# Optimization experiments

Hardware: AMD Instinct MI355X
Metric: run time of the kernel (lower is better)

## Reference

```python
import jax, jax.numpy as jnp
import numpy as np

DIM = 768
NUM_HEADS = 12
HEAD_DIM = DIM // NUM_HEADS
MAX_H = 32
MAX_W = 32


def setup_inputs() -> dict:
    key = jax.random.key(0)
    ks = jax.random.split(key, 7)
    B, H, W = 2, MAX_H, MAX_W
    N = H * W
    x = jax.random.normal(ks[0], (B, N, DIM), dtype=jnp.float32)
    qkv_w = jax.random.normal(ks[1], (3 * DIM, DIM), dtype=jnp.float32) * 0.02
    qkv_b = jax.random.normal(ks[2], (3 * DIM,), dtype=jnp.float32) * 0.02
    proj_w = jax.random.normal(ks[3], (DIM, DIM), dtype=jnp.float32) * 0.02
    proj_b = jax.random.normal(ks[4], (DIM,), dtype=jnp.float32) * 0.02
    rel_pos_h = jax.random.normal(ks[5], (2 * MAX_H - 1, HEAD_DIM), dtype=jnp.float32) * 0.02
    rel_pos_w = jax.random.normal(ks[6], (2 * MAX_W - 1, HEAD_DIM), dtype=jnp.float32) * 0.02
    return {"x": x, "qkv_w": qkv_w, "qkv_b": qkv_b, "proj_w": proj_w,
            "proj_b": proj_b, "rel_pos_h": rel_pos_h, "rel_pos_w": rel_pos_w,
            "x_h": H, "x_w": W}


def _rel_index(q_size, k_size):
    # q_size == k_size here (x_hw == max_hw), ratios are 1 and _interpolate is identity
    dist = jnp.arange(q_size)[:, None] - jnp.arange(k_size)[None, :] + (k_size - 1)
    return dist  # values in [0, 2*k_size-2]


def reference(x, qkv_w, qkv_b, proj_w, proj_b, rel_pos_h, rel_pos_w, x_h, x_w):
    B, N, dim = x.shape
    nh, hd = NUM_HEADS, HEAD_DIM
    qkv = (x @ qkv_w.T + qkv_b).reshape(B, N, 3, nh, hd)
    q, k, v = qkv[:, :, 0], qkv[:, :, 1], qkv[:, :, 2]  # [B, N, nh, hd]

    Rh = rel_pos_h[_rel_index(x_h, x_h)]  # [qh, kh, hd]
    Rw = rel_pos_w[_rel_index(x_w, x_w)]  # [qw, kw, hd]
    q2d = q.reshape(B, x_h, x_w, nh, hd)
    rel_h = jnp.einsum('bhwnc,hkc->bnhwk', q2d, Rh)  # [B, nh, qh, qw, kh]
    rel_w = jnp.einsum('bhwnc,wkc->bnhwk', q2d, Rw)  # [B, nh, qh, qw, kw]
    bias = (rel_h[..., :, None] + rel_w[..., None, :]).reshape(B, nh, N, N)

    scale = 1.0 / np.sqrt(hd).astype(np.float32)
    scores = jnp.einsum('bqhd,bkhd->bhqk', q, k) * scale + bias
    attn = jax.nn.softmax(scores, axis=-1)
    out = jnp.einsum('bhqk,bkhd->bqhd', attn, v).reshape(B, N, dim)
    return out @ proj_w.T + proj_b
```

## Files before the change

### kernel.cpp

```cpp
#include <hip/hip_runtime.h>

typedef float fx4 __attribute__((ext_vector_type(4)));
typedef float fx2 __attribute__((ext_vector_type(2)));
typedef short bfrag __attribute__((ext_vector_type(8)));
typedef float ffrag __attribute__((ext_vector_type(4)));
typedef unsigned short ush;

#define NTOK  1024
#define NHEADS 12
#define HD    64
#define DIMM  768

__device__ __forceinline__ float b2f(ush u) {
  union { unsigned i; float f; } x; x.i = ((unsigned)u) << 16; return x.f;
}
__device__ __forceinline__ ush f2b(float f) {
  union { float f; unsigned i; } x; x.f = f;
  unsigned r = x.i + 0x7fff + ((x.i >> 16) & 1);
  return (ush)(r >> 16);
}

__device__ __forceinline__ void gload16(const void* g, void* l) {
  __builtin_amdgcn_global_load_lds(
      (const __attribute__((address_space(1))) unsigned*)g,
      (__attribute__((address_space(3))) unsigned*)l, 16, 0, 0);
}

__device__ __forceinline__ ffrag mfma16(bfrag a, bfrag b, ffrag c) {
  return __builtin_amdgcn_mfma_f32_16x16x32_bf16(a, b, c, 0, 0, 0);
}

template<int N> __device__ __forceinline__ void vwait() {
  if constexpr (N == 0)      asm volatile("s_waitcnt vmcnt(0)" ::: "memory");
  else if constexpr (N == 1) asm volatile("s_waitcnt vmcnt(1)" ::: "memory");
  else if constexpr (N == 2) asm volatile("s_waitcnt vmcnt(2)" ::: "memory");
  else if constexpr (N == 3) asm volatile("s_waitcnt vmcnt(3)" ::: "memory");
  else if constexpr (N == 4) asm volatile("s_waitcnt vmcnt(4)" ::: "memory");
  else if constexpr (N == 6) asm volatile("s_waitcnt vmcnt(6)" ::: "memory");
  else if constexpr (N == 8) asm volatile("s_waitcnt vmcnt(8)" ::: "memory");
  else                       asm volatile("s_waitcnt vmcnt(12)" ::: "memory");
}
__device__ __forceinline__ void bar() {
  asm volatile("" ::: "memory");
  __builtin_amdgcn_s_barrier();
  asm volatile("" ::: "memory");
}
__device__ __forceinline__ void barL() {
  asm volatile("s_waitcnt lgkmcnt(0)" ::: "memory");
  __builtin_amdgcn_s_barrier();
  asm volatile("" ::: "memory");
}

__device__ __forceinline__ int swz(int row, int b) {
  return row * 128 + (b ^ ((row & 7) << 4));
}

__global__ __launch_bounds__(256) void k_cvt3(
    const float* __restrict__ x, const float* __restrict__ w,
    const float* __restrict__ pw,
    ush* __restrict__ xh, ush* __restrict__ xl,
    ush* __restrict__ wh,
    ush* __restrict__ pwh, ush* __restrict__ pwl)
{
  int i = blockIdx.x * 256 + threadIdx.x;
  const float* src; ush *h, *l; int off;
  bool wlo = true;
  if (i < 393216)      { src = x;  h = xh;  l = xl;  off = i; }
  else if (i < 835584) { src = w;  h = wh;  l = nullptr; wlo = false; off = i - 393216; }
  else                 { src = pw; h = pwh; l = pwl; off = i - 835584; }
  fx4 v = *(const fx4*)(src + (size_t)off * 4);
  ushort4 hh, ll;
  float t;
  hh.x = f2b(v[0]); t = v[0] - b2f(hh.x); ll.x = f2b(t);
  hh.y = f2b(v[1]); t = v[1] - b2f(hh.y); ll.y = f2b(t);
  hh.z = f2b(v[2]); t = v[2] - b2f(hh.z); ll.z = f2b(t);
  hh.w = f2b(v[3]); t = v[3] - b2f(hh.w); ll.w = f2b(t);
  *(ushort4*)(h + (size_t)off * 4) = hh;
  if (wlo) *(ushort4*)(l + (size_t)off * 4) = ll;
}

template<int MR, int NR, int NTERM>
__device__ __forceinline__ void gemm_pipe(
    const ush* __restrict__ Ah, const ush* __restrict__ Al,
    const ush* __restrict__ Bh, const ush* __restrict__ Bl,
    int row0, int col0, int K, short* lds, ffrag (&acc)[MR][NR])
{
  constexpr int F = (NTERM == 3) ? 4 * (MR + NR) : (4 * MR + 2 * NR);
  constexpr int LPS = F / 4;
  static_assert(F % 4 == 0, "frag count must be divisible by wave count");
  const int tid = threadIdx.x;
  const int lane = tid & 63, w = tid >> 6;
  const int wr = w >> 1, wc = w & 1;
  const int l15 = lane & 15, l8 = (lane >> 4) * 8;

  auto stage = [&](short* buf, int k0) {
    #pragma unroll
    for (int i = 0; i < LPS; i++) {
      int f = i * 4 + w;
      const ush* src;
      if (f < 2 * MR)
        src = Ah + (size_t)(row0 + f * 16 + l15) * K + k0 + l8;
      else if (f < 4 * MR)
        src = Al + (size_t)(row0 + (f - 2 * MR) * 16 + l15) * K + k0 + l8;
      else if (f < 4 * MR + 2 * NR)
        src = Bh + (size_t)(col0 + (f - 4 * MR) * 16 + l15) * K + k0 + l8;
      else
        src = Bl + (size_t)(col0 + (f - 4 * MR - 2 * NR) * 16 + l15) * K + k0 + l8;
      gload16(src, buf + f * 512);
    }
  };

  auto step = [&](const short* buf) {
    bfrag ah[MR], al[MR], bh[NR];
    #pragma unroll
    for (int i = 0; i < MR; i++) {
      ah[i] = *(const bfrag*)(buf + (wr * MR + i) * 512 + lane * 8);
      al[i] = *(const bfrag*)(buf + (2 * MR + wr * MR + i) * 512 + lane * 8);
    }
    #pragma unroll
    for (int j = 0; j < NR; j++)
      bh[j] = *(const bfrag*)(buf + (4 * MR + wc * NR + j) * 512 + lane * 8);
    if constexpr (NTERM == 3) {
      bfrag bl[NR];
      #pragma unroll
      for (int j = 0; j < NR; j++)
        bl[j] = *(const bfrag*)(buf + (4 * MR + 2 * NR + wc * NR + j) * 512 + lane * 8);
      #pragma unroll
      for (int i = 0; i < MR; i++)
        #pragma unroll
        for (int j = 0; j < NR; j++) {
          acc[i][j] = mfma16(ah[i], bh[j], acc[i][j]);
          acc[i][j] = mfma16(ah[i], bl[j], acc[i][j]);
          acc[i][j] = mfma16(al[i], bh[j], acc[i][j]);
        }
    } else {
      #pragma unroll
      for (int i = 0; i < MR; i++)
        #pragma unroll
        for (int j = 0; j < NR; j++) {
          acc[i][j] = mfma16(ah[i], bh[j], acc[i][j]);
          acc[i][j] = mfma16(al[i], bh[j], acc[i][j]);
        }
    }
  };

  const int nt = K / 32;
  stage(lds, 0);
  for (int t = 0; t < nt; t++) {
    bar();
    if (t + 1 < nt) {
      stage(lds + ((t + 1) & 1) * F * 512, (t + 1) * 32);
      vwait<LPS>();
    } else {
      vwait<0>();
    }
    bar();
    step(lds + (t & 1) * F * 512);
  }
}

__global__ __launch_bounds__(256) void k_qkv_mfma(
    const ush* __restrict__ xh, const ush* __restrict__ xl,
    const ush* __restrict__ wh,
    const float* __restrict__ bias,
    ush* __restrict__ qo, ush* __restrict__ ko, ush* __restrict__ vo)
{
  __shared__ short lds[2 * 24 * 512];
  const int orig = blockIdx.x;
  const int xcd = orig & 7, local = orig >> 3;
  const int lm = local & 3, ln = local >> 2;
  const int bm = (xcd & 3) * 4 + lm;
  const int bn = (xcd >> 2) * 9 + ln;
  const int row0 = bm * 128, col0 = bn * 128;
  ffrag acc[4][4] = {};
  gemm_pipe<4, 4, 2>(xh, xl, wh, wh, row0, col0, 768, lds, acc);

  const int tid = threadIdx.x, lane = tid & 63, w = tid >> 6;
  const int wr = w >> 1, wc = w & 1;
  const int l15 = lane & 15, l4 = lane >> 4;
  const int which = col0 / 768;
  const int base_head = (col0 - which * 768) >> 6;
  const int head = base_head + wc;
  ush* base = which == 0 ? qo : (which == 1 ? ko : vo);
  #pragma unroll
  for (int mi = 0; mi < 4; mi++)
    #pragma unroll
    for (int ni = 0; ni < 4; ni++) {
      int d = ni * 16 + l15;
      float bv = bias[col0 + wc * 64 + d];
      #pragma unroll
      for (int r = 0; r < 4; r++) {
        int row = row0 + wr * 64 + mi * 16 + l4 * 4 + r;
        int bb = row >> 10, n = row & 1023;
        base[((size_t)(bb * NHEADS + head) * NTOK + n) * HD + d] =
            f2b(acc[mi][ni][r] + bv);
      }
    }
}

__global__ __launch_bounds__(256) void k_proj_mfma(
    const ush* __restrict__ ah, const ush* __restrict__ al,
    const ush* __restrict__ bh, const ush* __restrict__ bl,
    const float* __restrict__ bias, float* __restrict__ out)
{
  __shared__ short lds[2 * 16 * 512];
  const int orig = blockIdx.x;
  const int xcd = orig & 7, local = orig >> 3;
  const int lm = local & 7, ln = local >> 3;
  const int bm = (xcd & 3) * 8 + lm;
  const int bn = (xcd >> 2) * 6 + ln;
  const int row0 = bm * 64, col0 = bn * 64;
  ffrag acc[2][2] = {};
  gemm_pipe<2, 2, 3>(ah, al, bh, bl, row0, col0, 768, lds, acc);

  const int tid = threadIdx.x, lane = tid & 63, w = tid >> 6;
  const int wr = w >> 1, wc = w & 1;
  const int l15 = lane & 15, l4 = lane >> 4;
  #pragma unroll
  for (int mi = 0; mi < 2; mi++)
    #pragma unroll
    for (int ni = 0; ni < 2; ni++) {
      int col = col0 + wc * 32 + ni * 16 + l15;
      float bv = bias[col];
      #pragma unroll
      for (int r = 0; r < 4; r++) {
        int row = row0 + wr * 32 + mi * 16 + l4 * 4 + r;
        out[(size_t)row * 768 + col] = acc[mi][ni][r] + bv;
      }
    }
}

__global__ __launch_bounds__(256) void k_rel(
    const ush* __restrict__ qT, const float* __restrict__ rph,
    const float* __restrict__ rpw,
    float* __restrict__ relh, float* __restrict__ relw)
{
  __shared__ float Qs[32][68];
  __shared__ float RhS[32][68];
  __shared__ float RwS[63][68];
  const int bid = blockIdx.x;
  const int pair = bid >> 5;
  const int nt = bid & 31;
  const int nbase = nt * 32;
  const ush* qp = qT + (size_t)pair * NTOK * HD + (size_t)nbase * HD;
  const int tid = threadIdx.x;
  #pragma unroll
  for (int ii = 0; ii < 2; ii++) {
    int f = ii * 256 + tid;
    int r = f >> 4, k4 = f & 15;
    ushort4 t = *(const ushort4*)(qp + (size_t)r * HD + k4 * 4);
    Qs[r][k4*4+0] = b2f(t.x); Qs[r][k4*4+1] = b2f(t.y);
    Qs[r][k4*4+2] = b2f(t.z); Qs[r][k4*4+3] = b2f(t.w);
    *(fx4*)&RhS[r][k4*4] = *(const fx4*)(rph + (size_t)(nt + r) * 64 + k4 * 4);
  }
  #pragma unroll
  for (int ii = 0; ii < 4; ii++) {
    int f = ii * 256 + tid;
    if (f < 1008) {
      int r = f >> 4, k4 = f & 15;
      *(fx4*)&RwS[r][k4*4] = *(const fx4*)(rpw + (size_t)r * 64 + k4 * 4);
    }
  }
  __syncthreads();
  const int nl = tid >> 3, rem = tid & 7;
  #pragma unroll
  for (int rep = 0; rep < 8; rep++) {
    int kidx = rep * 8 + rem;
    int hw = kidx >> 5;
    int k = kidx & 31;
    const float* rrow = hw ? &RwS[nl + 31 - k][0] : &RhS[31 - k][0];
    float sum = 0.f;
    #pragma unroll
    for (int c4 = 0; c4 < 16; c4++) {
      fx4 q = *(const fx4*)&Qs[nl][c4*4];
      fx4 rv = *(const fx4*)&rrow[c4*4];
      sum = fmaf(q[0], rv[0], sum);
      sum = fmaf(q[1], rv[1], sum);
      sum = fmaf(q[2], rv[2], sum);
      sum = fmaf(q[3], rv[3], sum);
    }
    float* dst = (hw ? relw : relh) + (size_t)pair * NTOK * 32 + (size_t)(nbase + nl) * 32 + k;
    *dst = sum;
  }
}

__global__ __launch_bounds__(256, 3) void k_attn_mfma(
    const ush* __restrict__ qT, const ush* __restrict__ kT,
    const ush* __restrict__ vT,
    const float* __restrict__ relh, const float* __restrict__ relw,
    ush* __restrict__ oph, ush* __restrict__ opl, float* __restrict__ ml)
{
  __shared__ short Kf[2 * 8 * 512];
  __shared__ char VTb[8192];
  __shared__ char Phb[8192];
  __shared__ char Plb[8192];
  __shared__ float RhS[64][36];

  const int orig = blockIdx.x;
  const int bid = (orig & 7) * 96 + (orig >> 3);
  const int ks   = bid & 1;
  const int qt   = (bid >> 1) & 15;
  const int pair = bid >> 5;
  const int q0 = qt * 64;
  const ush* qp = qT + (size_t)pair * NTOK * HD;
  const ush* kp = kT + (size_t)pair * NTOK * HD;
  const ush* vp = vT + (size_t)pair * NTOK * HD;
  const float* rhp = relh + (size_t)pair * NTOK * 32;
  const float* rwp = relw + (size_t)pair * NTOK * 32;

  const int tid = threadIdx.x;
  const int lane = tid & 63, w = tid >> 6;
  const int l15 = lane & 15, l4 = lane >> 4;
  const int wq = w * 16;
  const int kv = tid & 63, db = tid >> 6;

  auto issueK = [&](int tt) {
    const int gt = ks * 8 + tt;
    const ush* s0 = kp + (size_t)(gt * 64 + wq + l15) * HD + l4 * 8;
    short* dst = Kf + (tt & 1) * 4096 + (w * 2) * 512;
    gload16(s0, dst);
    gload16(s0 + 32, dst + 512);
  };
  auto issueV = [&](int tt, ushort4 (&vr)[4]) {
    const int gt = ks * 8 + tt;
    #pragma unroll
    for (int j = 0; j < 4; j++)
      vr[j] = *(const ushort4*)(vp + (size_t)(gt * 64 + kv) * HD + db * 16 + j * 4);
  };
  auto writeVT = [&](ushort4 (&vr)[4]) {
    #pragma unroll
    for (int j = 0; j < 4; j++) {
      int d0 = db * 16 + j * 4;
      *(ush*)(VTb + swz(d0 + 0, 2 * kv)) = vr[j].x;
      *(ush*)(VTb + swz(d0 + 1, 2 * kv)) = vr[j].y;
      *(ush*)(VTb + swz(d0 + 2, 2 * kv)) = vr[j].z;
      *(ush*)(VTb + swz(d0 + 3, 2 * kv)) = vr[j].w;
    }
  };

  {
    int row = tid >> 2, seg = tid & 3;
    const float* src = rhp + (size_t)(q0 + row) * 32 + seg * 8;
    *(fx4*)&RhS[row][seg * 8]     = *(const fx4*)src;
    *(fx4*)&RhS[row][seg * 8 + 4] = *(const fx4*)(src + 4);
  }
  bfrag qf[2];
  qf[0] = *(const bfrag*)(qp + (size_t)(q0 + wq + l15) * HD + l4 * 8);
  qf[1] = *(const bfrag*)(qp + (size_t)(q0 + wq + l15) * HD + 32 + l4 * 8);
  float rw[4][2];
  #pragma unroll
  for (int r = 0; r < 4; r++)
    #pragma unroll
    for (int h = 0; h < 2; h++)
      rw[r][h] = rwp[(size_t)(q0 + wq + l4 * 4 + r) * 32 + h * 16 + l15];

  asm volatile("" ::: "memory");
  ushort4 vrA[4], vrB[4];
  issueK(0); issueV(0, vrA); issueV(1, vrB);

  ffrag o[4] = {};
  float mrow[4] = {-3e38f, -3e38f, -3e38f, -3e38f};
  float lrow[4] = {};

  for (int tt = 0; tt < 8; tt++) {
    const int t = ks * 8 + tt;
    if (tt < 7) vwait<4>(); else vwait<0>();
    barL();

    if ((tt & 1) == 0) {
      writeVT(vrA);
      if (tt < 7) issueK(tt + 1);
      if (tt < 6) issueV(tt + 2, vrA);
    } else {
      writeVT(vrB);
      if (tt < 7) issueK(tt + 1);
      if (tt < 6) issueV(tt + 2, vrB);
    }

    const short* kbuf = Kf + (tt & 1) * 4096;
    ffrag s[4] = {};
    #pragma unroll
    for (int kf = 0; kf < 4; kf++) {
      bfrag kf0 = *(const bfrag*)(kbuf + (kf * 2 + 0) * 512 + lane * 8);
      bfrag kf1 = *(const bfrag*)(kbuf + (kf * 2 + 1) * 512 + lane * 8);
      s[kf] = mfma16(qf[0], kf0, s[kf]);
      s[kf] = mfma16(qf[1], kf1, s[kf]);
    }

    fx2 rh2[4];
    #pragma unroll
    for (int r = 0; r < 4; r++)
      rh2[r] = *(const fx2*)&RhS[wq + l4 * 4 + r][2 * t];
    float pm[4] = {-3e38f, -3e38f, -3e38f, -3e38f};
    #pragma unroll
    for (int kf = 0; kf < 4; kf++)
      #pragma unroll
      for (int r = 0; r < 4; r++) {
        float sc = fmaf(s[kf][r], 0.125f, rh2[r][kf >> 1] + rw[r][kf & 1]);
        s[kf][r] = sc;
        pm[r] = fmaxf(pm[r], sc);
      }
    #pragma unroll
    for (int off = 1; off < 16; off <<= 1)
      #pragma unroll
      for (int r = 0; r < 4; r++)
        pm[r] = fmaxf(pm[r], __shfl_xor(pm[r], off));
    float al[4], ps[4] = {0.f, 0.f, 0.f, 0.f};
    #pragma unroll
    for (int r = 0; r < 4; r++) {
      float mnew = fmaxf(mrow[r], pm[r]);
      al[r] = __expf(mrow[r] - mnew);
      mrow[r] = mnew;
    }
    #pragma unroll
    for (int kf = 0; kf < 4; kf++)
      #pragma unroll
      for (int r = 0; r < 4; r++) {
        float p = __expf(s[kf][r] - mrow[r]);
        s[kf][r] = p;
        ps[r] += p;
      }
    #pragma unroll
    for (int off = 1; off < 16; off <<= 1)
      #pragma unroll
      for (int r = 0; r < 4; r++)
        ps[r] += __shfl_xor(ps[r], off);
    #pragma unroll
    for (int r = 0; r < 4; r++)
      lrow[r] = fmaf(lrow[r], al[r], ps[r]);

    #pragma unroll
    for (int kf = 0; kf < 4; kf++)
      #pragma unroll
      for (int r = 0; r < 4; r++) {
        ush hi = f2b(s[kf][r]);
        float lo = s[kf][r] - b2f(hi);
        int a = swz(wq + l4 * 4 + r, kf * 32 + 2 * l15);
        *(ush*)(Phb + a) = hi;
        *(ush*)(Plb + a) = f2b(lo);
      }
    #pragma unroll
    for (int df = 0; df < 4; df++)
      #pragma unroll
      for (int r = 0; r < 4; r++)
        o[df][r] *= al[r];

    barL();

    bfrag ph[2], pl[2];
    #pragma unroll
    for (int kc = 0; kc < 2; kc++) {
      int a = swz(wq + l15, kc * 64 + l4 * 16);
      ph[kc] = *(const bfrag*)(Phb + a);
      pl[kc] = *(const bfrag*)(Plb + a);
    }
    #pragma unroll
    for (int df = 0; df < 4; df++)
      #pragma unroll
      for (int kc = 0; kc < 2; kc++) {
        bfrag vf = *(const bfrag*)(VTb + swz(df * 16 + l15, kc * 64 + l4 * 16));
        o[df] = mfma16(ph[kc], vf, o[df]);
        o[df] = mfma16(pl[kc], vf, o[df]);
      }
  }

  const int part = ((pair << 4) | qt) * 2 + ks;
  if (l15 == 0) {
    float* mlp = ml + (size_t)part * 128;
    #pragma unroll
    for (int r = 0; r < 4; r++) {
      int row = wq + l4 * 4 + r;
      mlp[row] = mrow[r];
      mlp[64 + row] = lrow[r];
    }
  }
  const size_t pbase = (size_t)part * 4096;
  #pragma unroll
  for (int df = 0; df < 4; df++)
    #pragma unroll
    for (int r = 0; r < 4; r++) {
      float val = o[df][r];
      int row = wq + l4 * 4 + r;
      size_t idx = pbase + (size_t)row * 64 + df * 16 + l15;
      ush hi = f2b(val);
      oph[idx] = hi;
      opl[idx] = f2b(val - b2f(hi));
    }
}

__global__ __launch_bounds__(256) void k_attn_merge(
    const ush* __restrict__ oph, const ush* __restrict__ opl,
    const float* __restrict__ ml,
    ush* __restrict__ o1h, ush* __restrict__ o1l)
{
  const int pq = blockIdx.x;
  const int pair = pq >> 4, qt = pq & 15;
  const int bb = pair / NHEADS, head = pair % NHEADS;
  __shared__ float M0[64], L0[64], M1[64], L1[64];
  const int tid = threadIdx.x;
  const float* mlp = ml + (size_t)pq * 256;
  if (tid < 64) {
    M0[tid] = mlp[tid];        L0[tid] = mlp[64 + tid];
    M1[tid] = mlp[128 + tid];  L1[tid] = mlp[192 + tid];
  }
  __syncthreads();
  const size_t b0 = (size_t)(pq * 2) * 4096;
  const size_t b1 = b0 + 4096;
  #pragma unroll
  for (int e = 0; e < 4; e++) {
    int q4 = e * 256 + tid;
    int row = q4 >> 4;
    int d4 = (q4 & 15) * 4;
    float m0 = M0[row], l0v = L0[row], m1 = M1[row], l1v = L1[row];
    float m = fmaxf(m0, m1);
    float a0 = __expf(m0 - m), a1 = __expf(m1 - m);
    float inv = 1.0f / (l0v * a0 + l1v * a1);
    ushort4 h0 = *(const ushort4*)(oph + b0 + (size_t)q4 * 4);
    ushort4 g0 = *(const ushort4*)(opl + b0 + (size_t)q4 * 4);
    ushort4 h1 = *(const ushort4*)(oph + b1 + (size_t)q4 * 4);
    ushort4 g1 = *(const ushort4*)(opl + b1 + (size_t)q4 * 4);
    float v0 = ((b2f(h0.x)+b2f(g0.x))*a0 + (b2f(h1.x)+b2f(g1.x))*a1) * inv;
    float v1 = ((b2f(h0.y)+b2f(g0.y))*a0 + (b2f(h1.y)+b2f(g1.y))*a1) * inv;
    float v2 = ((b2f(h0.z)+b2f(g0.z))*a0 + (b2f(h1.z)+b2f(g1.z))*a1) * inv;
    float v3 = ((b2f(h0.w)+b2f(g0.w))*a0 + (b2f(h1.w)+b2f(g1.w))*a1) * inv;
    size_t gidx = ((size_t)(bb * NTOK + qt * 64 + row)) * DIMM + head * HD + d4;
    ushort4 oh, ol;
    oh.x = f2b(v0); ol.x = f2b(v0 - b2f(oh.x));
    oh.y = f2b(v1); ol.y = f2b(v1 - b2f(oh.y));
    oh.z = f2b(v2); ol.z = f2b(v2 - b2f(oh.z));
    oh.w = f2b(v3); ol.w = f2b(v3 - b2f(oh.w));
    *(ushort4*)(o1h + gidx) = oh;
    *(ushort4*)(o1l + gidx) = ol;
  }
}

extern "C" void kernel_launch(void* const* d_in, const int* in_sizes, int n_in,
                              void* d_out, int out_size, void* d_ws, size_t ws_size,
                              hipStream_t stream)
{
  const float* x      = (const float*)d_in[0];
  const float* qkv_w  = (const float*)d_in[1];
  const float* qkv_b  = (const float*)d_in[2];
  const float* proj_w = (const float*)d_in[3];
  const float* proj_b = (const float*)d_in[4];
  const float* rph    = (const float*)d_in[5];
  const float* rpw    = (const float*)d_in[6];

  char* p = (char*)d_ws;
  ush* xh  = (ush*)p; p += 3145728;
  ush* xl  = (ush*)p; p += 3145728;
  ush* wh  = (ush*)p; p += 3538944;
  ush* wl  = (ush*)p; p += 3538944;
  ush* pwh = (ush*)p; p += 1179648;
  ush* pwl = (ush*)p; p += 1179648;
  ush* qb  = (ush*)p; p += 3145728;
  ush* kb  = (ush*)p; p += 3145728;
  ush* vb  = (ush*)p; p += 3145728;
  float* relh = (float*)p; p += 3145728;
  float* relw = (float*)p; p += 3145728;
  float* ml   = (float*)p; p += 393216;
  (void)wl;
  ush* oph = xh;
  ush* opl = wh;
  ush* o1h = qb;
  ush* o1l = kb;
  float* out = (float*)d_out;

  k_cvt3<<<dim3(3840), dim3(256), 0, stream>>>(x, qkv_w, proj_w,
                                               xh, xl, wh, pwh, pwl);
  k_qkv_mfma<<<dim3(288), dim3(256), 0, stream>>>(xh, xl, wh, qkv_b, qb, kb, vb);
  k_rel<<<dim3(768), dim3(256), 0, stream>>>(qb, rph, rpw, relh, relw);
  k_attn_mfma<<<dim3(768), dim3(256), 0, stream>>>(qb, kb, vb, relh, relw, oph, opl, ml);
  k_attn_merge<<<dim3(384), dim3(256), 0, stream>>>(oph, opl, ml, o1h, o1l);
  k_proj_mfma<<<dim3(384), dim3(256), 0, stream>>>(o1h, o1l, pwh, pwl, proj_b, out);
}
```

Before: 120.9 us.

## Replace LDS-staged GEMM pipeline with direct global-to-register double buffering

Removes the shared-memory staging and barriers from the QKV and projection GEMMs. Each wave now loads its own MFMA fragments straight from global memory into registers, double-buffered across K steps. This drops LDS traffic and the two barriers per step. In exchange, operand data that waves previously shared through LDS is now fetched redundantly from global memory or L2, and register pressure rises.

```diff
diff --git a/kernel.cpp b/kernel.cpp
--- a/kernel.cpp
+++ b/kernel.cpp
@@ -31,14 +31,10 @@
 }
 
 template<int N> __device__ __forceinline__ void vwait() {
-  if constexpr (N == 0)      asm volatile("s_waitcnt vmcnt(0)" ::: "memory");
-  else if constexpr (N == 1) asm volatile("s_waitcnt vmcnt(1)" ::: "memory");
-  else if constexpr (N == 2) asm volatile("s_waitcnt vmcnt(2)" ::: "memory");
-  else if constexpr (N == 3) asm volatile("s_waitcnt vmcnt(3)" ::: "memory");
-  else if constexpr (N == 4) asm volatile("s_waitcnt vmcnt(4)" ::: "memory");
-  else if constexpr (N == 6) asm volatile("s_waitcnt vmcnt(6)" ::: "memory");
-  else if constexpr (N == 8) asm volatile("s_waitcnt vmcnt(8)" ::: "memory");
-  else                       asm volatile("s_waitcnt vmcnt(12)" ::: "memory");
+  if constexpr (N == 0)       asm volatile("s_waitcnt vmcnt(0)" ::: "memory");
+  else if constexpr (N == 4)  asm volatile("s_waitcnt vmcnt(4)" ::: "memory");
+  else if constexpr (N == 6)  asm volatile("s_waitcnt vmcnt(6)" ::: "memory");
+  else                        asm volatile("s_waitcnt vmcnt(8)" ::: "memory");
 }
 __device__ __forceinline__ void bar() {
   asm volatile("" ::: "memory");
@@ -79,152 +75,136 @@
   if (wlo) *(ushort4*)(l + (size_t)off * 4) = ll;
 }
 
-template<int MR, int NR, int NTERM>
-__device__ __forceinline__ void gemm_pipe(
-    const ush* __restrict__ Ah, const ush* __restrict__ Al,
-    const ush* __restrict__ Bh, const ush* __restrict__ Bl,
-    int row0, int col0, int K, short* lds, ffrag (&acc)[MR][NR])
-{
-  constexpr int F = (NTERM == 3) ? 4 * (MR + NR) : (4 * MR + 2 * NR);
-  constexpr int LPS = F / 4;
-  static_assert(F % 4 == 0, "frag count must be divisible by wave count");
-  const int tid = threadIdx.x;
-  const int lane = tid & 63, w = tid >> 6;
-  const int wr = w >> 1, wc = w & 1;
-  const int l15 = lane & 15, l8 = (lane >> 4) * 8;
-
-  auto stage = [&](short* buf, int k0) {
-    #pragma unroll
-    for (int i = 0; i < LPS; i++) {
-      int f = i * 4 + w;
-      const ush* src;
-      if (f < 2 * MR)
-        src = Ah + (size_t)(row0 + f * 16 + l15) * K + k0 + l8;
-      else if (f < 4 * MR)
-        src = Al + (size_t)(row0 + (f - 2 * MR) * 16 + l15) * K + k0 + l8;
-      else if (f < 4 * MR + 2 * NR)
-        src = Bh + (size_t)(col0 + (f - 4 * MR) * 16 + l15) * K + k0 + l8;
-      else
-        src = Bl + (size_t)(col0 + (f - 4 * MR - 2 * NR) * 16 + l15) * K + k0 + l8;
-      gload16(src, buf + f * 512);
-    }
-  };
-
-  auto step = [&](const short* buf) {
-    bfrag ah[MR], al[MR], bh[NR];
-    #pragma unroll
-    for (int i = 0; i < MR; i++) {
-      ah[i] = *(const bfrag*)(buf + (wr * MR + i) * 512 + lane * 8);
-      al[i] = *(const bfrag*)(buf + (2 * MR + wr * MR + i) * 512 + lane * 8);
-    }
-    #pragma unroll
-    for (int j = 0; j < NR; j++)
-      bh[j] = *(const bfrag*)(buf + (4 * MR + wc * NR + j) * 512 + lane * 8);
-    if constexpr (NTERM == 3) {
-      bfrag bl[NR];
-      #pragma unroll
-      for (int j = 0; j < NR; j++)
-        bl[j] = *(const bfrag*)(buf + (4 * MR + 2 * NR + wc * NR + j) * 512 + lane * 8);
-      #pragma unroll
-      for (int i = 0; i < MR; i++)
-        #pragma unroll
-        for (int j = 0; j < NR; j++) {
-          acc[i][j] = mfma16(ah[i], bh[j], acc[i][j]);
-          acc[i][j] = mfma16(ah[i], bl[j], acc[i][j]);
-          acc[i][j] = mfma16(al[i], bh[j], acc[i][j]);
-        }
-    } else {
-      #pragma unroll
-      for (int i = 0; i < MR; i++)
-        #pragma unroll
-        for (int j = 0; j < NR; j++) {
-          acc[i][j] = mfma16(ah[i], bh[j], acc[i][j]);
-          acc[i][j] = mfma16(al[i], bh[j], acc[i][j]);
-        }
-    }
-  };
-
-  const int nt = K / 32;
-  stage(lds, 0);
-  for (int t = 0; t < nt; t++) {
-    bar();
-    if (t + 1 < nt) {
-      stage(lds + ((t + 1) & 1) * F * 512, (t + 1) * 32);
-      vwait<LPS>();
-    } else {
-      vwait<0>();
-    }
-    bar();
-    step(lds + (t & 1) * F * 512);
-  }
-}
-
 __global__ __launch_bounds__(256) void k_qkv_mfma(
     const ush* __restrict__ xh, const ush* __restrict__ xl,
     const ush* __restrict__ wh,
     const float* __restrict__ bias,
     ush* __restrict__ qo, ush* __restrict__ ko, ush* __restrict__ vo)
 {
-  __shared__ short lds[2 * 24 * 512];
   const int orig = blockIdx.x;
   const int xcd = orig & 7, local = orig >> 3;
   const int lm = local & 3, ln = local >> 2;
   const int bm = (xcd & 3) * 4 + lm;
   const int bn = (xcd >> 2) * 9 + ln;
-  const int row0 = bm * 128, col0 = bn * 128;
-  ffrag acc[4][4] = {};
-  gemm_pipe<4, 4, 2>(xh, xl, wh, wh, row0, col0, 768, lds, acc);
-
   const int tid = threadIdx.x, lane = tid & 63, w = tid >> 6;
   const int wr = w >> 1, wc = w & 1;
+  const int row0 = bm * 128 + wr * 64;
+  const int col0 = bn * 128 + wc * 64;
   const int l15 = lane & 15, l4 = lane >> 4;
+  const int K = 768;
+
+  const ush* pa[4]; const ush* pl[4]; const ush* pb[4];
+  #pragma unroll
+  for (int i = 0; i < 4; i++) {
+    size_t ro = (size_t)(row0 + i * 16 + l15) * K + l4 * 8;
+    size_t co = (size_t)(col0 + i * 16 + l15) * K + l4 * 8;
+    pa[i] = xh + ro; pl[i] = xl + ro; pb[i] = wh + co;
+  }
+
+  bfrag A0[4], L0[4], B0[4], A1[4], L1[4], B1[4];
+  ffrag acc[4][4] = {};
+
+#define LOADQ(A, L, B)                                          \
+  { _Pragma("unroll") for (int i = 0; i < 4; i++) {             \
+      A[i] = *(const bfrag*)pa[i]; pa[i] += 32;                 \
+      L[i] = *(const bfrag*)pl[i]; pl[i] += 32;                 \
+      B[i] = *(const bfrag*)pb[i]; pb[i] += 32; } }
+#define STEPQ(A, L, B)                                          \
+  { _Pragma("unroll") for (int i = 0; i < 4; i++)               \
+      _Pragma("unroll") for (int j = 0; j < 4; j++) {           \
+        acc[i][j] = mfma16(A[i], B[j], acc[i][j]);              \
+        acc[i][j] = mfma16(L[i], B[j], acc[i][j]); } }
+
+  LOADQ(A0, L0, B0);
+  for (int t = 0; t < 24; t += 2) {
+    LOADQ(A1, L1, B1);
+    STEPQ(A0, L0, B0);
+    if (t + 2 < 24) LOADQ(A0, L0, B0);
+    STEPQ(A1, L1, B1);
+  }
+#undef LOADQ
+#undef STEPQ
+
   const int which = col0 / 768;
-  const int base_head = (col0 - which * 768) >> 6;
-  const int head = base_head + wc;
-  ush* base = which == 0 ? qo : (which == 1 ? ko : vo);
+  const int head  = (col0 - which * 768) >> 6;
+  ush* basep = which == 0 ? qo : (which == 1 ? ko : vo);
   #pragma unroll
   for (int mi = 0; mi < 4; mi++)
     #pragma unroll
     for (int ni = 0; ni < 4; ni++) {
       int d = ni * 16 + l15;
-      float bv = bias[col0 + wc * 64 + d];
+      float bv = bias[col0 + d];
       #pragma unroll
       for (int r = 0; r < 4; r++) {
-        int row = row0 + wr * 64 + mi * 16 + l4 * 4 + r;
+        int row = row0 + mi * 16 + l4 * 4 + r;
         int bb = row >> 10, n = row & 1023;
-        base[((size_t)(bb * NHEADS + head) * NTOK + n) * HD + d] =
+        basep[((size_t)(bb * NHEADS + head) * NTOK + n) * HD + d] =
             f2b(acc[mi][ni][r] + bv);
       }
     }
 }
 
 __global__ __launch_bounds__(256) void k_proj_mfma(
-    const ush* __restrict__ ah, const ush* __restrict__ al,
-    const ush* __restrict__ bh, const ush* __restrict__ bl,
+    const ush* __restrict__ ah_, const ush* __restrict__ al_,
+    const ush* __restrict__ bh_, const ush* __restrict__ bl_,
     const float* __restrict__ bias, float* __restrict__ out)
 {
-  __shared__ short lds[2 * 16 * 512];
   const int orig = blockIdx.x;
   const int xcd = orig & 7, local = orig >> 3;
   const int lm = local & 7, ln = local >> 3;
   const int bm = (xcd & 3) * 8 + lm;
   const int bn = (xcd >> 2) * 6 + ln;
-  const int row0 = bm * 64, col0 = bn * 64;
-  ffrag acc[2][2] = {};
-  gemm_pipe<2, 2, 3>(ah, al, bh, bl, row0, col0, 768, lds, acc);
-
   const int tid = threadIdx.x, lane = tid & 63, w = tid >> 6;
   const int wr = w >> 1, wc = w & 1;
+  const int row0 = bm * 64 + wr * 32;
+  const int col0 = bn * 64 + wc * 32;
   const int l15 = lane & 15, l4 = lane >> 4;
+  const int K = 768;
+
+  const ush *pah[2], *pal[2], *pbh[2], *pbl[2];
+  #pragma unroll
+  for (int i = 0; i < 2; i++) {
+    size_t ro = (size_t)(row0 + i * 16 + l15) * K + l4 * 8;
+    size_t co = (size_t)(col0 + i * 16 + l15) * K + l4 * 8;
+    pah[i] = ah_ + ro; pal[i] = al_ + ro;
+    pbh[i] = bh_ + co; pbl[i] = bl_ + co;
+  }
+
+  bfrag A0[2], L0[2], B0[2], C0[2], A1[2], L1[2], B1[2], C1[2];
+  ffrag acc[2][2] = {};
+
+#define LOADP(A, L, B, C)                                       \
+  { _Pragma("unroll") for (int i = 0; i < 2; i++) {             \
+      A[i] = *(const bfrag*)pah[i]; pah[i] += 32;               \
+      L[i] = *(const bfrag*)pal[i]; pal[i] += 32;               \
+      B[i] = *(const bfrag*)pbh[i]; pbh[i] += 32;               \
+      C[i] = *(const bfrag*)pbl[i]; pbl[i] += 32; } }
+#define STEPP(A, L, B, C)                                       \
+  { _Pragma("unroll") for (int i = 0; i < 2; i++)               \
+      _Pragma("unroll") for (int j = 0; j < 2; j++) {           \
+        acc[i][j] = mfma16(A[i], B[j], acc[i][j]);              \
+        acc[i][j] = mfma16(A[i], C[j], acc[i][j]);              \
+        acc[i][j] = mfma16(L[i], B[j], acc[i][j]); } }
+
+  LOADP(A0, L0, B0, C0);
+  for (int t = 0; t < 24; t += 2) {
+    LOADP(A1, L1, B1, C1);
+    STEPP(A0, L0, B0, C0);
+    if (t + 2 < 24) LOADP(A0, L0, B0, C0);
+    STEPP(A1, L1, B1, C1);
+  }
+#undef LOADP
+#undef STEPP
+
   #pragma unroll
   for (int mi = 0; mi < 2; mi++)
     #pragma unroll
     for (int ni = 0; ni < 2; ni++) {
-      int col = col0 + wc * 32 + ni * 16 + l15;
+      int col = col0 + ni * 16 + l15;
       float bv = bias[col];
       #pragma unroll
       for (int r = 0; r < 4; r++) {
-        int row = row0 + wr * 32 + mi * 16 + l4 * 4 + r;
+        int row = row0 + mi * 16 + l4 * 4 + r;
         out[(size_t)row * 768 + col] = acc[mi][ni][r] + bv;
       }
     }
```

Result: slower. 172.4 us (+42.5%).

## Fuse relative-position bias computation into attention kernel using MFMA

Applied to the files above, without the earlier changes.

Removes the separate k_rel kernel and its fp32 relh/relw buffers in global memory. Each attention block now computes its rel_h and rel_w bias terms directly with bf16 MFMA, using a hi/lo split of the rel_pos tables that the conversion kernel now produces. Phb/Plb are reused as scratch for the rel_w gather before the main loop. This saves one kernel launch and the buffer round trip, but adds redundant per-block MFMA work, and both split attention blocks of each query tile compute the same bias.

```diff
diff --git a/kernel.cpp b/kernel.cpp
--- a/kernel.cpp
+++ b/kernel.cpp
@@ -31,14 +31,10 @@
 }
 
 template<int N> __device__ __forceinline__ void vwait() {
-  if constexpr (N == 0)      asm volatile("s_waitcnt vmcnt(0)" ::: "memory");
-  else if constexpr (N == 1) asm volatile("s_waitcnt vmcnt(1)" ::: "memory");
-  else if constexpr (N == 2) asm volatile("s_waitcnt vmcnt(2)" ::: "memory");
-  else if constexpr (N == 3) asm volatile("s_waitcnt vmcnt(3)" ::: "memory");
-  else if constexpr (N == 4) asm volatile("s_waitcnt vmcnt(4)" ::: "memory");
-  else if constexpr (N == 6) asm volatile("s_waitcnt vmcnt(6)" ::: "memory");
-  else if constexpr (N == 8) asm volatile("s_waitcnt vmcnt(8)" ::: "memory");
-  else                       asm volatile("s_waitcnt vmcnt(12)" ::: "memory");
+  if constexpr (N == 0)       asm volatile("s_waitcnt vmcnt(0)" ::: "memory");
+  else if constexpr (N == 4)  asm volatile("s_waitcnt vmcnt(4)" ::: "memory");
+  else if constexpr (N == 6)  asm volatile("s_waitcnt vmcnt(6)" ::: "memory");
+  else                        asm volatile("s_waitcnt vmcnt(8)" ::: "memory");
 }
 __device__ __forceinline__ void bar() {
   asm volatile("" ::: "memory");
@@ -57,17 +53,23 @@
 
 __global__ __launch_bounds__(256) void k_cvt3(
     const float* __restrict__ x, const float* __restrict__ w,
-    const float* __restrict__ pw,
+    const float* __restrict__ pw, const float* __restrict__ rph,
+    const float* __restrict__ rpw,
     ush* __restrict__ xh, ush* __restrict__ xl,
     ush* __restrict__ wh,
-    ush* __restrict__ pwh, ush* __restrict__ pwl)
+    ush* __restrict__ pwh, ush* __restrict__ pwl,
+    ush* __restrict__ rphh, ush* __restrict__ rphl,
+    ush* __restrict__ rpwh, ush* __restrict__ rpwl)
 {
   int i = blockIdx.x * 256 + threadIdx.x;
+  if (i >= 985056) return;
   const float* src; ush *h, *l; int off;
-  bool wlo = true;
+  bool lo = true;
   if (i < 393216)      { src = x;  h = xh;  l = xl;  off = i; }
-  else if (i < 835584) { src = w;  h = wh;  l = nullptr; wlo = false; off = i - 393216; }
-  else                 { src = pw; h = pwh; l = pwl; off = i - 835584; }
+  else if (i < 835584) { src = w;  h = wh;  l = nullptr; lo = false; off = i - 393216; }
+  else if (i < 983040) { src = pw; h = pwh; l = pwl; off = i - 835584; }
+  else if (i < 984048) { src = rph; h = rphh; l = rphl; off = i - 983040; }
+  else                 { src = rpw; h = rpwh; l = rpwl; off = i - 984048; }
   fx4 v = *(const fx4*)(src + (size_t)off * 4);
   ushort4 hh, ll;
   float t;
@@ -76,7 +78,7 @@
   hh.z = f2b(v[2]); t = v[2] - b2f(hh.z); ll.z = f2b(t);
   hh.w = f2b(v[3]); t = v[3] - b2f(hh.w); ll.w = f2b(t);
   *(ushort4*)(h + (size_t)off * 4) = hh;
-  if (wlo) *(ushort4*)(l + (size_t)off * 4) = ll;
+  if (lo) *(ushort4*)(l + (size_t)off * 4) = ll;
 }
 
 template<int MR, int NR, int NTERM>
@@ -230,71 +232,18 @@
     }
 }
 
-__global__ __launch_bounds__(256) void k_rel(
-    const ush* __restrict__ qT, const float* __restrict__ rph,
-    const float* __restrict__ rpw,
-    float* __restrict__ relh, float* __restrict__ relw)
-{
-  __shared__ float Qs[32][68];
-  __shared__ float RhS[32][68];
-  __shared__ float RwS[63][68];
-  const int bid = blockIdx.x;
-  const int pair = bid >> 5;
-  const int nt = bid & 31;
-  const int nbase = nt * 32;
-  const ush* qp = qT + (size_t)pair * NTOK * HD + (size_t)nbase * HD;
-  const int tid = threadIdx.x;
-  #pragma unroll
-  for (int ii = 0; ii < 2; ii++) {
-    int f = ii * 256 + tid;
-    int r = f >> 4, k4 = f & 15;
-    ushort4 t = *(const ushort4*)(qp + (size_t)r * HD + k4 * 4);
-    Qs[r][k4*4+0] = b2f(t.x); Qs[r][k4*4+1] = b2f(t.y);
-    Qs[r][k4*4+2] = b2f(t.z); Qs[r][k4*4+3] = b2f(t.w);
-    *(fx4*)&RhS[r][k4*4] = *(const fx4*)(rph + (size_t)(nt + r) * 64 + k4 * 4);
-  }
-  #pragma unroll
-  for (int ii = 0; ii < 4; ii++) {
-    int f = ii * 256 + tid;
-    if (f < 1008) {
-      int r = f >> 4, k4 = f & 15;
-      *(fx4*)&RwS[r][k4*4] = *(const fx4*)(rpw + (size_t)r * 64 + k4 * 4);
-    }
-  }
-  __syncthreads();
-  const int nl = tid >> 3, rem = tid & 7;
-  #pragma unroll
-  for (int rep = 0; rep < 8; rep++) {
-    int kidx = rep * 8 + rem;
-    int hw = kidx >> 5;
-    int k = kidx & 31;
-    const float* rrow = hw ? &RwS[nl + 31 - k][0] : &RhS[31 - k][0];
-    float sum = 0.f;
-    #pragma unroll
-    for (int c4 = 0; c4 < 16; c4++) {
-      fx4 q = *(const fx4*)&Qs[nl][c4*4];
-      fx4 rv = *(const fx4*)&rrow[c4*4];
-      sum = fmaf(q[0], rv[0], sum);
-      sum = fmaf(q[1], rv[1], sum);
-      sum = fmaf(q[2], rv[2], sum);
-      sum = fmaf(q[3], rv[3], sum);
-    }
-    float* dst = (hw ? relw : relh) + (size_t)pair * NTOK * 32 + (size_t)(nbase + nl) * 32 + k;
-    *dst = sum;
-  }
-}
-
 __global__ __launch_bounds__(256, 3) void k_attn_mfma(
     const ush* __restrict__ qT, const ush* __restrict__ kT,
     const ush* __restrict__ vT,
-    const float* __restrict__ relh, const float* __restrict__ relw,
+    const ush* __restrict__ rphh, const ush* __restrict__ rphl,
+    const ush* __restrict__ rpwh, const ush* __restrict__ rpwl,
     ush* __restrict__ oph, ush* __restrict__ opl, float* __restrict__ ml)
 {
   __shared__ short Kf[2 * 8 * 512];
   __shared__ char VTb[8192];
   __shared__ char Phb[8192];
   __shared__ char Plb[8192];
-  __shared__ float RhS[64][36];
+  __shared__ float RhS[64][34];
 
   const int orig = blockIdx.x;
   const int bid = (orig & 7) * 96 + (orig >> 3);
@@ -305,8 +254,6 @@
   const ush* qp = qT + (size_t)pair * NTOK * HD;
   const ush* kp = kT + (size_t)pair * NTOK * HD;
   const ush* vp = vT + (size_t)pair * NTOK * HD;
-  const float* rhp = relh + (size_t)pair * NTOK * 32;
-  const float* rwp = relw + (size_t)pair * NTOK * 32;
 
   const int tid = threadIdx.x;
   const int lane = tid & 63, w = tid >> 6;
@@ -338,21 +285,71 @@
     }
   };
 
-  {
-    int row = tid >> 2, seg = tid & 3;
-    const float* src = rhp + (size_t)(q0 + row) * 32 + seg * 8;
-    *(fx4*)&RhS[row][seg * 8]     = *(const fx4*)src;
-    *(fx4*)&RhS[row][seg * 8 + 4] = *(const fx4*)(src + 4);
-  }
   bfrag qf[2];
   qf[0] = *(const bfrag*)(qp + (size_t)(q0 + wq + l15) * HD + l4 * 8);
   qf[1] = *(const bfrag*)(qp + (size_t)(q0 + wq + l15) * HD + 32 + l4 * 8);
+
+  {
+    const int qh = (q0 + wq) >> 5;
+    #pragma unroll
+    for (int kb = 0; kb < 2; kb++) {
+      int rrow = qh + 31 - (kb * 16 + l15);
+      const ush* bh = rphh + rrow * 64 + l4 * 8;
+      const ush* bl = rphl + rrow * 64 + l4 * 8;
+      bfrag b0 = *(const bfrag*)bh;
+      bfrag b1 = *(const bfrag*)(bh + 32);
+      bfrag c0 = *(const bfrag*)bl;
+      bfrag c1 = *(const bfrag*)(bl + 32);
+      ffrag s = {};
+      s = mfma16(qf[0], b0, s);
+      s = mfma16(qf[1], b1, s);
+      s = mfma16(qf[0], c0, s);
+      s = mfma16(qf[1], c1, s);
+      #pragma unroll
+      for (int r = 0; r < 4; r++)
+        RhS[wq + l4 * 4 + r][kb * 16 + l15] = s[r];
+    }
+  }
+
   float rw[4][2];
-  #pragma unroll
-  for (int r = 0; r < 4; r++)
-    #pragma unroll
-    for (int h = 0; h < 2; h++)
-      rw[r][h] = rwp[(size_t)(q0 + wq + l4 * 4 + r) * 32 + h * 16 + l15];
+  {
+    #pragma unroll
+    for (int dbk = 0; dbk < 4; dbk++) {
+      int rrow = dbk * 16 + l15;
+      const ush* bh = rpwh + rrow * 64 + l4 * 8;
+      const ush* bl = rpwl + rrow * 64 + l4 * 8;
+      bfrag b0 = *(const bfrag*)bh;
+      bfrag b1 = *(const bfrag*)(bh + 32);
+      bfrag c0 = *(const bfrag*)bl;
+      bfrag c1 = *(const bfrag*)(bl + 32);
+      ffrag s = {};
+      s = mfma16(qf[0], b0, s);
+      s = mfma16(qf[1], b1, s);
+      s = mfma16(qf[0], c0, s);
+      s = mfma16(qf[1], c1, s);
+      #pragma unroll
+      for (int r = 0; r < 4; r++) {
+        int row = l4 * 4 + r, d = dbk * 16 + l15;
+        float* dst = (d < 32)
+          ? (float*)(Phb + (wq + row) * 128 + (d & 31) * 4)
+          : (float*)(Plb + (wq + row) * 128 + (d & 31) * 4);
+        *dst = s[r];
+      }
+    }
+    #pragma unroll
+    for (int r = 0; r < 4; r++) {
+      int row = l4 * 4 + r;
+      int qw = (q0 + wq + row) & 31;
+      #pragma unroll
+      for (int h = 0; h < 2; h++) {
+        int d = qw + 31 - (h * 16 + l15);
+        const float* srcp = (d < 32)
+          ? (const float*)(Phb + (wq + row) * 128 + (d & 31) * 4)
+          : (const float*)(Plb + (wq + row) * 128 + (d & 31) * 4);
+        rw[r][h] = *srcp;
+      }
+    }
+  }
 
   asm volatile("" ::: "memory");
   ushort4 vrA[4], vrB[4];
@@ -556,9 +553,11 @@
   ush* qb  = (ush*)p; p += 3145728;
   ush* kb  = (ush*)p; p += 3145728;
   ush* vb  = (ush*)p; p += 3145728;
-  float* relh = (float*)p; p += 3145728;
-  float* relw = (float*)p; p += 3145728;
-  float* ml   = (float*)p; p += 393216;
+  float* ml = (float*)p; p += 393216;
+  ush* rphh = (ush*)p; p += 8192;
+  ush* rphl = (ush*)p; p += 8192;
+  ush* rpwh = (ush*)p; p += 8192;
+  ush* rpwl = (ush*)p; p += 8192;
   (void)wl;
   ush* oph = xh;
   ush* opl = wh;
@@ -566,11 +565,13 @@
   ush* o1l = kb;
   float* out = (float*)d_out;
 
-  k_cvt3<<<dim3(3840), dim3(256), 0, stream>>>(x, qkv_w, proj_w,
-                                               xh, xl, wh, pwh, pwl);
+  k_cvt3<<<dim3(3849), dim3(256), 0, stream>>>(x, qkv_w, proj_w, rph, rpw,
+                                               xh, xl, wh, pwh, pwl,
+                                               rphh, rphl, rpwh, rpwl);
   k_qkv_mfma<<<dim3(288), dim3(256), 0, stream>>>(xh, xl, wh, qkv_b, qb, kb, vb);
-  k_rel<<<dim3(768), dim3(256), 0, stream>>>(qb, rph, rpw, relh, relw);
-  k_attn_mfma<<<dim3(768), dim3(256), 0, stream>>>(qb, kb, vb, relh, relw, oph, opl, ml);
+  k_attn_mfma<<<dim3(768), dim3(256), 0, stream>>>(qb, kb, vb,
+                                                   rphh, rphl, rpwh, rpwl,
+                                                   oph, opl, ml);
   k_attn_merge<<<dim3(384), dim3(256), 0, stream>>>(oph, opl, ml, o1h, o1l);
   k_proj_mfma<<<dim3(384), dim3(256), 0, stream>>>(o1h, o1l, pwh, pwl, proj_b, out);
 }
```

Result: no change. 119.4 us (-1.2%).
